# Performance work log

Hardware: AMD Instinct MI355X
Metric: run time of the kernel (lower is better)

## Reference

```python
import jax, jax.numpy as jnp
import numpy as np

B, S, D, H = 4, 2048, 1024, 16
HD = D // H
QMIN, QMAX = -128.0, 127.0


def fq(x):
    """Int8 per-tensor fake-quant (quantize-dequantize), straight-through."""
    s = jnp.maximum(jnp.max(jnp.abs(x)) / QMAX, 1e-8)
    q = jnp.clip(jnp.round(x / s), QMIN, QMAX) * s
    return x + jax.lax.stop_gradient(q - x)


def layernorm(x, g, b):
    m = jnp.mean(x, axis=-1, keepdims=True)
    v = jnp.var(x, axis=-1, keepdims=True)
    return (x - m) * jax.lax.rsqrt(v + 1e-5) * g + b


def rope(x):
    # x: [B, H, S, HD]; rotate-half RoPE
    half = HD // 2
    inv = 1.0 / (10000.0 ** (jnp.arange(half, dtype=jnp.float32) / half))
    ang = jnp.arange(S, dtype=jnp.float32)[:, None] * inv[None, :]  # [S, half]
    cos, sin = jnp.cos(ang), jnp.sin(ang)
    x1, x2 = x[..., :half], x[..., half:]
    return jnp.concatenate([x1 * cos - x2 * sin, x1 * sin + x2 * cos], axis=-1)


def setup_inputs() -> dict:
    key = jax.random.key(0)
    ks = jax.random.split(key, 16)
    w = lambda k, shp: jax.random.normal(k, shp, dtype=jnp.float32) * 0.02
    return {
        "x": jax.random.normal(ks[0], (B, S, D), dtype=jnp.float32),
        "g1": jnp.ones((D,), jnp.float32), "bn1": jnp.zeros((D,), jnp.float32),
        "Wq": w(ks[1], (D, D)), "bq": jnp.zeros((D,), jnp.float32),
        "Wk": w(ks[2], (D, D)), "bk": jnp.zeros((D,), jnp.float32),
        "Wv": w(ks[3], (D, D)), "bv": jnp.zeros((D,), jnp.float32),
        "Wo": w(ks[4], (D, D)), "bo": jnp.zeros((D,), jnp.float32),
        "g2": jnp.ones((D,), jnp.float32), "bn2": jnp.zeros((D,), jnp.float32),
        "W1": w(ks[5], (4 * D, D)), "bf1": jnp.zeros((4 * D,), jnp.float32),
        "W2": w(ks[6], (D, 4 * D)), "bf2": jnp.zeros((D,), jnp.float32),
    }


def reference(x, g1, bn1, Wq, bq, Wk, bk, Wv, bv, Wo, bo, g2, bn2, W1, bf1, W2, bf2):
    # --- attention branch: LN -> int8 quant -> RoPE MHSA -> quant add ---
    residual = x
    h = fq(layernorm(x, g1, bn1))  # post_norm1_quant
    q = h @ fq(Wq).T + bq
    k = h @ fq(Wk).T + bk
    v = h @ fq(Wv).T + bv
    q = rope(q.reshape(B, S, H, HD).transpose(0, 2, 1, 3))
    k = rope(k.reshape(B, S, H, HD).transpose(0, 2, 1, 3))
    v = v.reshape(B, S, H, HD).transpose(0, 2, 1, 3)
    scores = jnp.einsum("bhqd,bhkd->bhqk", q, k) / np.sqrt(HD).astype(np.float32)
    attn = jax.nn.softmax(scores, axis=-1)
    o = jnp.einsum("bhqk,bhkd->bhqd", attn, v)
    o = o.transpose(0, 2, 1, 3).reshape(B, S, D)
    o = fq(o @ fq(Wo).T + bo)  # attn returns quant tensor
    x = fq(o + residual)       # QuantAdd
    # --- MLP branch: LN -> quant -> fc1 -> GELU -> quant -> fc2 -> quant add ---
    residual = x
    h = fq(layernorm(x, g2, bn2))  # post_norm2_quant
    h = h @ fq(W1).T + bf1
    h = jax.nn.gelu(h, approximate=False)
    h = fq(h)                       # post_gelu_quant
    h = h @ fq(W2).T + bf2
    return fq(h + residual)         # QuantAdd
```

## Files before the change

### kernel.cpp

```cpp
#include <hip/hip_runtime.h>
#include <math.h>

#define Bdim 4
#define Sdim 2048
#define Ddim 1024
#define Hdim 16
#define HDdim 64

typedef unsigned long long u64;
typedef unsigned short ushort_t;
typedef int int4v __attribute__((ext_vector_type(4)));
typedef short short8v __attribute__((ext_vector_type(8)));
typedef float float4v __attribute__((ext_vector_type(4)));
typedef unsigned short us4v __attribute__((ext_vector_type(4)));

__device__ __forceinline__ float qdq_f(float x, float amax) {
  float s = fmaxf(amax / 127.0f, 1e-8f);
  float r = rintf(x / s);
  r = fminf(fmaxf(r, -128.0f), 127.0f);
  return r * s;
}

__device__ __forceinline__ void atomicMaxF(float* a, float v) {
  atomicMax((int*)a, __float_as_int(v));
}

__device__ __forceinline__ float blockMax256(float v) {
  __shared__ float sred[4];
  #pragma unroll
  for (int o = 32; o > 0; o >>= 1) v = fmaxf(v, __shfl_xor(v, o));
  if ((threadIdx.x & 63) == 0) sred[threadIdx.x >> 6] = v;
  __syncthreads();
  return fmaxf(fmaxf(sred[0], sred[1]), fmaxf(sred[2], sred[3]));
}

__device__ __forceinline__ ushort_t f2bf(float f) {
  unsigned u = __float_as_uint(f);
  return (ushort_t)((u + 0x7FFFu + ((u >> 16) & 1u)) >> 16);
}
__device__ __forceinline__ float bf2f(ushort_t h) {
  return __uint_as_float(((unsigned)h) << 16);
}

__global__ void init_scalars(float* s) { s[threadIdx.x] = 0.0f; }

__global__ __launch_bounds__(256) void absmax6_kernel(
    const float* __restrict__ Wq, const float* __restrict__ Wk,
    const float* __restrict__ Wv, const float* __restrict__ Wo,
    const float* __restrict__ W1, const float* __restrict__ W2,
    float* __restrict__ Sc)
{
  const u64 DD = (u64)Ddim * Ddim;
  int blk = blockIdx.x;
  const float* src; float* dst; u64 lb, nb, n;
  if (blk < 256)       { src = Wq; dst = Sc + 1; lb = blk;        nb = 256;  n = DD; }
  else if (blk < 512)  { src = Wk; dst = Sc + 2; lb = blk - 256;  nb = 256;  n = DD; }
  else if (blk < 768)  { src = Wv; dst = Sc + 3; lb = blk - 512;  nb = 256;  n = DD; }
  else if (blk < 1024) { src = Wo; dst = Sc + 4; lb = blk - 768;  nb = 256;  n = DD; }
  else if (blk < 2048) { src = W1; dst = Sc + 5; lb = blk - 1024; nb = 1024; n = 4 * DD; }
  else                 { src = W2; dst = Sc + 6; lb = blk - 2048; nb = 1024; n = 4 * DD; }
  u64 i = lb * 256 + threadIdx.x;
  u64 stride = nb * 256;
  float m = 0.0f;
  for (; i < n; i += stride) m = fmaxf(m, fabsf(src[i]));
  m = blockMax256(m);
  if (threadIdx.x == 0) atomicMaxF(dst, m);
}

__global__ __launch_bounds__(256) void quantw_kernel(
    const float* __restrict__ Wq, const float* __restrict__ Wk,
    const float* __restrict__ Wv, const float* __restrict__ Wo,
    const float* __restrict__ W1, const float* __restrict__ W2,
    signed char* __restrict__ Wq8, signed char* __restrict__ Wk8,
    signed char* __restrict__ Wv8, ushort_t* __restrict__ WoBF,
    signed char* __restrict__ W18, signed char* __restrict__ W28,
    const float* __restrict__ Sc)
{
  const u64 DD = (u64)Ddim * Ddim;
  int blk = blockIdx.x;
  if (blk < 2816) {
    const float* src; signed char* dst; float sa; u64 lb, nb, n4;
    if (blk < 256)       { src = Wq; dst = Wq8; sa = Sc[1]; lb = blk;        nb = 256;  n4 = DD / 4; }
    else if (blk < 512)  { src = Wk; dst = Wk8; sa = Sc[2]; lb = blk - 256;  nb = 256;  n4 = DD / 4; }
    else if (blk < 768)  { src = Wv; dst = Wv8; sa = Sc[3]; lb = blk - 512;  nb = 256;  n4 = DD / 4; }
    else if (blk < 1792) { src = W1; dst = W18; sa = Sc[5]; lb = blk - 768;  nb = 1024; n4 = DD; }
    else                 { src = W2; dst = W28; sa = Sc[6]; lb = blk - 1792; nb = 1024; n4 = DD; }
    const float s = fmaxf(sa / 127.0f, 1e-8f);
    u64 i = lb * 256 + threadIdx.x;
    u64 stride = nb * 256;
    for (; i < n4; i += stride) {
      float4 v = ((const float4*)src)[i];
      int b0 = (int)fminf(fmaxf(rintf(v.x / s), -128.0f), 127.0f) & 255;
      int b1 = (int)fminf(fmaxf(rintf(v.y / s), -128.0f), 127.0f) & 255;
      int b2 = (int)fminf(fmaxf(rintf(v.z / s), -128.0f), 127.0f) & 255;
      int b3 = (int)fminf(fmaxf(rintf(v.w / s), -128.0f), 127.0f) & 255;
      ((unsigned*)dst)[i] = (unsigned)(b0 | (b1 << 8) | (b2 << 16) | (b3 << 24));
    }
  } else {
    const float s = fmaxf(Sc[4] / 127.0f, 1e-8f);
    u64 i = (u64)(blk - 2816) * 256 + threadIdx.x;
    u64 stride = 1024ull * 256;
    for (; i < DD; i += stride) {
      float r = fminf(fmaxf(rintf(Wo[i] / s), -128.0f), 127.0f);
      WoBF[i] = f2bf(r);
    }
  }
}

__global__ __launch_bounds__(256) void quant8_kernel(
    const float* __restrict__ x, const float* __restrict__ amaxp,
    signed char* __restrict__ q, u64 n4)
{
  const float s = fmaxf(*amaxp / 127.0f, 1e-8f);
  u64 i = (u64)blockIdx.x * 256 + threadIdx.x;
  u64 stride = (u64)gridDim.x * 256;
  for (; i < n4; i += stride) {
    float4 v = ((const float4*)x)[i];
    int b0 = (int)fminf(fmaxf(rintf(v.x / s), -128.0f), 127.0f) & 255;
    int b1 = (int)fminf(fmaxf(rintf(v.y / s), -128.0f), 127.0f) & 255;
    int b2 = (int)fminf(fmaxf(rintf(v.z / s), -128.0f), 127.0f) & 255;
    int b3 = (int)fminf(fmaxf(rintf(v.w / s), -128.0f), 127.0f) & 255;
    ((unsigned*)q)[i] = (unsigned)(b0 | (b1 << 8) | (b2 << 16) | (b3 << 24));
  }
}

__global__ __launch_bounds__(256) void ln_kernel(
    const float* __restrict__ x, const float* __restrict__ g,
    const float* __restrict__ beta, const float* __restrict__ inAmax,
    float* __restrict__ y, float* __restrict__ amaxOut)
{
  __shared__ float sred[4];
  __shared__ float smv[2];
  const int tid = threadIdx.x;
  const u64 row = blockIdx.x;
  const float* xr = x + row * Ddim;
  float* yr = y + row * Ddim;
  float aIn = inAmax ? *inAmax : 0.0f;

  float vals[4];
  float sum = 0.0f;
  #pragma unroll
  for (int i = 0; i < 4; i++) {
    float v = xr[tid + (i << 8)];
    if (inAmax) v = qdq_f(v, aIn);
    vals[i] = v;
    sum += v;
  }
  #pragma unroll
  for (int o = 32; o > 0; o >>= 1) sum += __shfl_xor(sum, o);
  if ((tid & 63) == 0) sred[tid >> 6] = sum;
  __syncthreads();
  if (tid == 0) smv[0] = (sred[0] + sred[1] + sred[2] + sred[3]) * (1.0f / 1024.0f);
  __syncthreads();
  const float mean = smv[0];

  float dev = 0.0f;
  #pragma unroll
  for (int i = 0; i < 4; i++) { float d = vals[i] - mean; dev += d * d; }
  #pragma unroll
  for (int o = 32; o > 0; o >>= 1) dev += __shfl_xor(dev, o);
  if ((tid & 63) == 0) sred[tid >> 6] = dev;
  __syncthreads();
  if (tid == 0) {
    float var = (sred[0] + sred[1] + sred[2] + sred[3]) * (1.0f / 1024.0f);
    smv[1] = 1.0f / sqrtf(var + 1e-5f);
  }
  __syncthreads();
  const float inv = smv[1];

  float lmax = 0.0f;
  #pragma unroll
  for (int i = 0; i < 4; i++) {
    int c = tid + (i << 8);
    float ov = (vals[i] - mean) * inv * g[c] + beta[c];
    yr[c] = ov;
    lmax = fmaxf(lmax, fabsf(ov));
  }
  #pragma unroll
  for (int o = 32; o > 0; o >>= 1) lmax = fmaxf(lmax, __shfl_xor(lmax, o));
  __syncthreads();
  if ((tid & 63) == 0) sred[tid >> 6] = lmax;
  __syncthreads();
  if (tid == 0)
    atomicMaxF(amaxOut, fmaxf(fmaxf(sred[0], sred[1]), fmaxf(sred[2], sred[3])));
}

template <int EPI>
__global__ __launch_bounds__(256) void gemm_i8(
    const signed char* __restrict__ A8, const signed char* __restrict__ B8,
    const float* __restrict__ bias, float* __restrict__ C,
    int M, int N, int K,
    const float* __restrict__ sAp, const float* __restrict__ sBp,
    float* __restrict__ amaxOut,
    const float* __restrict__ Tm = nullptr,
    const float* __restrict__ amaxT = nullptr)
{
  __shared__ __align__(16) signed char As[128][80];
  __shared__ __align__(16) signed char Bs[128][80];
  const int tid = threadIdx.x;
  const int wave = tid >> 6, lane = tid & 63;
  const int quad = lane >> 4, l16 = lane & 15;
  const int wy = wave >> 1, wx = wave & 1;
  const int m0 = blockIdx.y << 7, n0 = blockIdx.x << 7;
  const float sA = fmaxf(*sAp / 127.0f, 1e-8f);
  const float sB = fmaxf(*sBp / 127.0f, 1e-8f);
  const float sAB = sA * sB;
  const float aT = (EPI == 2) ? *amaxT : 0.0f;

  const int sr = tid >> 2;
  const int sc = (tid & 3) << 4;

  int4v acc[4][4] = {};
  for (int k0 = 0; k0 < K; k0 += 64) {
    #pragma unroll
    for (int p = 0; p < 2; p++) {
      int r = sr + (p << 6);
      uint4 av = *(const uint4*)&A8[(u64)(m0 + r) * K + k0 + sc];
      uint4 bv = *(const uint4*)&B8[(u64)(n0 + r) * K + k0 + sc];
      *(uint4*)&As[r][sc] = av;
      *(uint4*)&Bs[r][sc] = bv;
    }
    __syncthreads();
    int4v af[4], bf[4];
    #pragma unroll
    for (int mt = 0; mt < 4; mt++)
      af[mt] = *(const int4v*)&As[(wy << 6) + (mt << 4) + l16][quad << 4];
    #pragma unroll
    for (int nt = 0; nt < 4; nt++)
      bf[nt] = *(const int4v*)&Bs[(wx << 6) + (nt << 4) + l16][quad << 4];
    #pragma unroll
    for (int mt = 0; mt < 4; mt++)
      #pragma unroll
      for (int nt = 0; nt < 4; nt++)
        acc[mt][nt] = __builtin_amdgcn_mfma_i32_16x16x64_i8(af[mt], bf[nt], acc[mt][nt], 0, 0, 0);
    __syncthreads();
  }

  float lmax = 0.0f;
  #pragma unroll
  for (int mt = 0; mt < 4; mt++) {
    #pragma unroll
    for (int reg = 0; reg < 4; reg++) {
      int row = m0 + (wy << 6) + (mt << 4) + (quad << 2) + reg;
      #pragma unroll
      for (int nt = 0; nt < 4; nt++) {
        int col = n0 + (wx << 6) + (nt << 4) + l16;
        float v = (float)acc[mt][nt][reg] * sAB + bias[col];
        if (EPI == 1) {
          v = 0.5f * v * (1.0f + erff(v * 0.70710678118654752440f));
          lmax = fmaxf(lmax, fabsf(v));
        }
        if (EPI == 2) {
          v += qdq_f(Tm[(u64)row * N + col], aT);
          lmax = fmaxf(lmax, fabsf(v));
        }
        C[(u64)row * N + col] = v;
      }
    }
  }
  if (EPI >= 1) {
    lmax = blockMax256(lmax);
    if (tid == 0) atomicMaxF(amaxOut, lmax);
  }
}

__global__ __launch_bounds__(256) void gemm_bf16_wo(
    const ushort_t* __restrict__ Ahi, const ushort_t* __restrict__ Alo,
    const ushort_t* __restrict__ Bw, const float* __restrict__ bias,
    float* __restrict__ C, int M, int N, int K,
    const float* __restrict__ sWp, float* __restrict__ amaxOut)
{
  __shared__ __align__(16) ushort_t Hs[128][40];
  __shared__ __align__(16) ushort_t Ls[128][40];
  __shared__ __align__(16) ushort_t Ws[128][40];
  const int tid = threadIdx.x;
  const int wave = tid >> 6, lane = tid & 63;
  const int quad = lane >> 4, l16 = lane & 15;
  const int wy = wave >> 1, wx = wave & 1;
  const int m0 = blockIdx.y << 7, n0 = blockIdx.x << 7;
  const float sW = fmaxf(*sWp / 127.0f, 1e-8f);

  const int sr = tid >> 2;
  const int sce = (tid & 3) << 3;

  float4v acc[4][4] = {};
  for (int k0 = 0; k0 < K; k0 += 32) {
    #pragma unroll
    for (int p = 0; p < 2; p++) {
      int r = sr + (p << 6);
      uint4 hv = *(const uint4*)&Ahi[(u64)(m0 + r) * K + k0 + sce];
      uint4 lv = *(const uint4*)&Alo[(u64)(m0 + r) * K + k0 + sce];
      uint4 wv = *(const uint4*)&Bw[(u64)(n0 + r) * K + k0 + sce];
      *(uint4*)&Hs[r][sce] = hv;
      *(uint4*)&Ls[r][sce] = lv;
      *(uint4*)&Ws[r][sce] = wv;
    }
    __syncthreads();
    short8v ah[4], al[4], bw[4];
    #pragma unroll
    for (int mt = 0; mt < 4; mt++) {
      ah[mt] = *(const short8v*)&Hs[(wy << 6) + (mt << 4) + l16][quad << 3];
      al[mt] = *(const short8v*)&Ls[(wy << 6) + (mt << 4) + l16][quad << 3];
    }
    #pragma unroll
    for (int nt = 0; nt < 4; nt++)
      bw[nt] = *(const short8v*)&Ws[(wx << 6) + (nt << 4) + l16][quad << 3];
    #pragma unroll
    for (int mt = 0; mt < 4; mt++)
      #pragma unroll
      for (int nt = 0; nt < 4; nt++) {
        acc[mt][nt] = __builtin_amdgcn_mfma_f32_16x16x32_bf16(ah[mt], bw[nt], acc[mt][nt], 0, 0, 0);
        acc[mt][nt] = __builtin_amdgcn_mfma_f32_16x16x32_bf16(al[mt], bw[nt], acc[mt][nt], 0, 0, 0);
      }
    __syncthreads();
  }

  float lmax = 0.0f;
  #pragma unroll
  for (int mt = 0; mt < 4; mt++) {
    #pragma unroll
    for (int reg = 0; reg < 4; reg++) {
      int row = m0 + (wy << 6) + (mt << 4) + (quad << 2) + reg;
      #pragma unroll
      for (int nt = 0; nt < 4; nt++) {
        int col = n0 + (wx << 6) + (nt << 4) + l16;
        float v = acc[mt][nt][reg] * sW + bias[col];
        lmax = fmaxf(lmax, fabsf(v));
        C[(u64)row * N + col] = v;
      }
    }
  }
  lmax = blockMax256(lmax);
  if (tid == 0) atomicMaxF(amaxOut, lmax);
}

__global__ __launch_bounds__(256) void prep_attn(
    const float* __restrict__ q, const float* __restrict__ k,
    const float* __restrict__ v,
    ushort_t* __restrict__ QH, ushort_t* __restrict__ QL,
    ushort_t* __restrict__ KH, ushort_t* __restrict__ KL,
    ushort_t* __restrict__ VTH, ushort_t* __restrict__ VTL,
    float* __restrict__ NQ, float* __restrict__ KMX)
{
  const int bh = blockIdx.y;
  const int b = bh >> 4, h = bh & 15;
  const int s0 = blockIdx.x << 6;
  const int tid = threadIdx.x;
  float kml = 0.0f;

  #pragma unroll
  for (int i = 0; i < 8; i++) {
    int idx = tid + (i << 8);
    int s = idx >> 5, hp = idx & 31;
    int sa = s0 + s;
    u64 gin = ((u64)(b * Sdim + sa) * Hdim + h) * HDdim + hp;
    float inv = powf(10000.0f, -(float)hp * (1.0f / 32.0f));
    float ang = (float)sa * inv;
    float cs = cosf(ang), sn = sinf(ang);
    float q1 = q[gin], q2 = q[gin + 32];
    float k1 = k[gin], k2 = k[gin + 32];
    float qo1 = (q1 * cs - q2 * sn) * 0.125f;
    float qo2 = (q1 * sn + q2 * cs) * 0.125f;
    float ko1 = k1 * cs - k2 * sn;
    float ko2 = k1 * sn + k2 * cs;
    u64 go = ((u64)bh * Sdim + sa) * HDdim + hp;
    ushort_t t;
    t = f2bf(qo1); QH[go]      = t; QL[go]      = f2bf(qo1 - bf2f(t));
    t = f2bf(qo2); QH[go + 32] = t; QL[go + 32] = f2bf(qo2 - bf2f(t));
    t = f2bf(ko1); KH[go]      = t; KL[go]      = f2bf(ko1 - bf2f(t));
    t = f2bf(ko2); KH[go + 32] = t; KL[go + 32] = f2bf(ko2 - bf2f(t));
    float nq2 = qo1 * qo1 + qo2 * qo2;
    float nk2 = ko1 * ko1 + ko2 * ko2;
    #pragma unroll
    for (int o = 16; o >= 1; o >>= 1) {
      nq2 += __shfl_xor(nq2, o);
      nk2 += __shfl_xor(nk2, o);
    }
    if (hp == 0) {
      NQ[(u64)bh * Sdim + sa] = sqrtf(nq2);
      kml = fmaxf(kml, sqrtf(nk2));
    }
  }
  kml = blockMax256(kml);
  if (tid == 0) atomicMaxF(&KMX[bh], kml);

  __shared__ ushort_t VHs[64][66], VLs[64][66];
  #pragma unroll
  for (int i = 0; i < 4; i++) {
    int idx4 = tid + (i << 8);
    int s = idx4 >> 4, c4 = (idx4 & 15) << 2;
    u64 gin = ((u64)(b * Sdim + s0 + s) * Hdim + h) * HDdim + c4;
    float4 vv = *(const float4*)&v[gin];
    float va[4] = {vv.x, vv.y, vv.z, vv.w};
    #pragma unroll
    for (int j = 0; j < 4; j++) {
      ushort_t vh = f2bf(va[j]);
      VHs[s][c4 + j] = vh;
      VLs[s][c4 + j] = f2bf(va[j] - bf2f(vh));
    }
  }
  __syncthreads();
  #pragma unroll
  for (int i = 0; i < 4; i++) {
    int idx4 = tid + (i << 8);
    int hd = idx4 >> 4, s4 = (idx4 & 15) << 2;
    us4v oh, ol;
    #pragma unroll
    for (int j = 0; j < 4; j++) { oh[j] = VHs[s4 + j][hd]; ol[j] = VLs[s4 + j][hd]; }
    u64 go = ((u64)bh * HDdim + hd) * Sdim + s0 + s4;
    *(us4v*)&VTH[go] = oh;
    *(us4v*)&VTL[go] = ol;
  }
}

__global__ __launch_bounds__(256) void attn_kernel(
    const ushort_t* __restrict__ QH, const ushort_t* __restrict__ QL,
    const ushort_t* __restrict__ KH, const ushort_t* __restrict__ KL,
    const ushort_t* __restrict__ VTH, const ushort_t* __restrict__ VTL,
    const float* __restrict__ NQ, const float* __restrict__ KMX,
    ushort_t* __restrict__ OHI, ushort_t* __restrict__ OLO)
{
  __shared__ __align__(16) ushort_t KHs[64][72], KLs[64][72];
  __shared__ __align__(16) ushort_t VHs[64][72], VLs[64][72];
  __shared__ __align__(16) float PF[128][68];
  const int tid = threadIdx.x;
  const int wave = tid >> 6, lane = tid & 63;
  const int quad = lane >> 4, l16 = lane & 15;
  const int w32 = wave << 5;
  const int bh = blockIdx.y;
  const int b = bh >> 4, h = bh & 15;
  const int q0 = blockIdx.x << 7;
  const u64 bhS = (u64)bh * Sdim;

  short8v qh[2][2], ql[2][2];
  #pragma unroll
  for (int mt = 0; mt < 2; mt++)
    #pragma unroll
    for (int kk = 0; kk < 2; kk++) {
      u64 g = (bhS + q0 + w32 + (mt << 4) + l16) * HDdim + (kk << 5) + (quad << 3);
      qh[mt][kk] = *(const short8v*)&QH[g];
      ql[mt][kk] = *(const short8v*)&QL[g];
    }

  const float kmax = KMX[bh] * 1.0009765625f;
  float Mb[2][4], lsum[2][4];
  #pragma unroll
  for (int mt = 0; mt < 2; mt++)
    #pragma unroll
    for (int r = 0; r < 4; r++) {
      Mb[mt][r] = NQ[bhS + q0 + w32 + (mt << 4) + (quad << 2) + r] * kmax;
      lsum[mt][r] = 0.0f;
    }

  float4v oacc[2][4] = {};

  for (int j0 = 0; j0 < Sdim; j0 += 64) {
    __syncthreads();
    #pragma unroll
    for (int i = 0; i < 2; i++) {
      int idx = tid + (i << 8);
      int r = idx >> 3, c8 = (idx & 7) << 3;
      u64 gk = (bhS + j0 + r) * HDdim + c8;
      *(uint4*)&KHs[r][c8] = *(const uint4*)&KH[gk];
      *(uint4*)&KLs[r][c8] = *(const uint4*)&KL[gk];
      u64 gv = ((u64)bh * HDdim + r) * Sdim + j0 + c8;
      *(uint4*)&VHs[r][c8] = *(const uint4*)&VTH[gv];
      *(uint4*)&VLs[r][c8] = *(const uint4*)&VTL[gv];
    }
    __syncthreads();

    float4v sc[2][4] = {};
    #pragma unroll
    for (int kk = 0; kk < 2; kk++)
      #pragma unroll
      for (int nt = 0; nt < 4; nt++) {
        short8v bh_ = *(const short8v*)&KHs[(nt << 4) + l16][(kk << 5) + (quad << 3)];
        short8v bl_ = *(const short8v*)&KLs[(nt << 4) + l16][(kk << 5) + (quad << 3)];
        #pragma unroll
        for (int mt = 0; mt < 2; mt++) {
          sc[mt][nt] = __builtin_amdgcn_mfma_f32_16x16x32_bf16(qh[mt][kk], bh_, sc[mt][nt], 0, 0, 0);
          sc[mt][nt] = __builtin_amdgcn_mfma_f32_16x16x32_bf16(qh[mt][kk], bl_, sc[mt][nt], 0, 0, 0);
          sc[mt][nt] = __builtin_amdgcn_mfma_f32_16x16x32_bf16(ql[mt][kk], bh_, sc[mt][nt], 0, 0, 0);
        }
      }

    #pragma unroll
    for (int mt = 0; mt < 2; mt++)
      #pragma unroll
      for (int r = 0; r < 4; r++) {
        int prow = w32 + (mt << 4) + (quad << 2) + r;
        float lacc = 0.0f;
        #pragma unroll
        for (int nt = 0; nt < 4; nt++) {
          float p = __expf(sc[mt][nt][r] - Mb[mt][r]);
          lacc += p;
          PF[prow][(nt << 4) + l16] = p;
        }
        lsum[mt][r] += lacc;
      }

    #pragma unroll
    for (int kk = 0; kk < 2; kk++) {
      short8v vh[4], vl[4];
      #pragma unroll
      for (int nt = 0; nt < 4; nt++) {
        vh[nt] = *(const short8v*)&VHs[(nt << 4) + l16][(kk << 5) + (quad << 3)];
        vl[nt] = *(const short8v*)&VLs[(nt << 4) + l16][(kk << 5) + (quad << 3)];
      }
      #pragma unroll
      for (int mt = 0; mt < 2; mt++) {
        const float* prp = &PF[w32 + (mt << 4) + l16][(kk << 5) + (quad << 3)];
        float4v pa = *(const float4v*)prp;
        float4v pb = *(const float4v*)(prp + 4);
        short8v ph, pl;
        #pragma unroll
        for (int j = 0; j < 4; j++) {
          unsigned ua = __float_as_uint(pa[j]);
          unsigned ub = __float_as_uint(pb[j]);
          float la = pa[j] - __uint_as_float(ua & 0xffff0000u);
          float lb = pb[j] - __uint_as_float(ub & 0xffff0000u);
          ph[j]     = (short)(ua >> 16);
          ph[4 + j] = (short)(ub >> 16);
          pl[j]     = (short)(__float_as_uint(la) >> 16);
          pl[4 + j] = (short)(__float_as_uint(lb) >> 16);
        }
        #pragma unroll
        for (int nt = 0; nt < 4; nt++) {
          oacc[mt][nt] = __builtin_amdgcn_mfma_f32_16x16x32_bf16(ph, vh[nt], oacc[mt][nt], 0, 0, 0);
          oacc[mt][nt] = __builtin_amdgcn_mfma_f32_16x16x32_bf16(ph, vl[nt], oacc[mt][nt], 0, 0, 0);
          oacc[mt][nt] = __builtin_amdgcn_mfma_f32_16x16x32_bf16(pl, vh[nt], oacc[mt][nt], 0, 0, 0);
        }
      }
    }
  }

  #pragma unroll
  for (int mt = 0; mt < 2; mt++)
    #pragma unroll
    for (int r = 0; r < 4; r++) {
      float l = lsum[mt][r];
      #pragma unroll
      for (int o = 8; o >= 1; o >>= 1) l += __shfl_xor(l, o);
      lsum[mt][r] = l;
    }

  #pragma unroll
  for (int mt = 0; mt < 2; mt++)
    #pragma unroll
    for (int r = 0; r < 4; r++) {
      float invl = 1.0f / lsum[mt][r];
      int srow = q0 + w32 + (mt << 4) + (quad << 2) + r;
      u64 gbase = ((u64)(b * Sdim + srow) * Hdim + h) * HDdim;
      #pragma unroll
      for (int nt = 0; nt < 4; nt++) {
        float o = oacc[mt][nt][r] * invl;
        ushort_t t = f2bf(o);
        OHI[gbase + (nt << 4) + l16] = t;
        OLO[gbase + (nt << 4) + l16] = f2bf(o - bf2f(t));
      }
    }
}

__global__ __launch_bounds__(256) void add_qdq_kernel(
    const float* __restrict__ a, const float* __restrict__ amaxA,
    const float* __restrict__ x, float* __restrict__ outp, u64 n,
    float* __restrict__ amaxOut)
{
  const float aA = *amaxA;
  u64 i = (u64)blockIdx.x * 256 + threadIdx.x;
  u64 stride = (u64)gridDim.x * 256;
  float m = 0.0f;
  for (; i < n; i += stride) {
    float t = qdq_f(a[i], aA) + x[i];
    outp[i] = t;
    m = fmaxf(m, fabsf(t));
  }
  m = blockMax256(m);
  if (threadIdx.x == 0) atomicMaxF(amaxOut, m);
}

__global__ __launch_bounds__(256) void qdq_out_kernel(
    const float* __restrict__ u, const float* __restrict__ amaxU,
    float* __restrict__ o, u64 n)
{
  const float aU = *amaxU;
  u64 i = (u64)blockIdx.x * 256 + threadIdx.x;
  u64 stride = (u64)gridDim.x * 256;
  for (; i < n; i += stride) o[i] = qdq_f(u[i], aU);
}

extern "C" void kernel_launch(void* const* d_in, const int* in_sizes, int n_in,
                              void* d_out, int out_size, void* d_ws, size_t ws_size,
                              hipStream_t stream)
{
  const float* x   = (const float*)d_in[0];
  const float* g1  = (const float*)d_in[1];
  const float* bn1 = (const float*)d_in[2];
  const float* Wq  = (const float*)d_in[3];
  const float* bq  = (const float*)d_in[4];
  const float* Wk  = (const float*)d_in[5];
  const float* bk  = (const float*)d_in[6];
  const float* Wv  = (const float*)d_in[7];
  const float* bv  = (const float*)d_in[8];
  const float* Wo  = (const float*)d_in[9];
  const float* bo  = (const float*)d_in[10];
  const float* g2  = (const float*)d_in[11];
  const float* bn2 = (const float*)d_in[12];
  const float* W1  = (const float*)d_in[13];
  const float* bf1 = (const float*)d_in[14];
  const float* W2  = (const float*)d_in[15];
  const float* bf2 = (const float*)d_in[16];
  float* out = (float*)d_out;

  const u64 NBSD = (u64)Bdim * Sdim * Ddim;
  const u64 NB4  = NBSD * 4;
  const u64 DD   = (u64)Ddim * Ddim;

  char* Wb = (char*)d_ws;
  float*       Sc   = (float*)Wb;
  float*       U0   = (float*)(Wb + 1024);
  float*       U1   = (float*)(Wb + 1024 + NB4);
  float*       F    = (float*)(Wb + 1024 + 2 * NB4);
  signed char* A8   = (signed char*)(Wb + 1024 + 6 * NB4);
  signed char* Wq8  = A8 + NBSD;
  signed char* Wk8  = Wq8 + DD;
  signed char* Wv8  = Wk8 + DD;
  signed char* W18  = Wv8 + DD;
  signed char* W28  = W18 + 4 * DD;
  ushort_t*    WoBF = (ushort_t*)(W28 + 4 * DD);
  float*       NQ   = (float*)(WoBF + DD);
  float*       KMX  = Sc + 128;

  float* F0 = F;
  float* F1 = F + NBSD;
  ushort_t* QHp = (ushort_t*)(F + 2 * NBSD);
  ushort_t* QLp = QHp + NBSD;
  ushort_t* KHp = (ushort_t*)(F + 3 * NBSD);
  ushort_t* KLp = KHp + NBSD;
  ushort_t* VTH = (ushort_t*)U0;
  ushort_t* VTL = VTH + NBSD;
  ushort_t* OHI = (ushort_t*)U1;
  ushort_t* OLO = OHI + NBSD;
  signed char* G8 = (signed char*)U0;

  const u64 needBytes = (u64)((char*)(NQ + (u64)64 * Sdim) - Wb);
  if (ws_size < needBytes) return;

  init_scalars<<<1, 256, 0, stream>>>(Sc);

  ln_kernel<<<Bdim * Sdim, 256, 0, stream>>>(x, g1, bn1, nullptr, U0, Sc + 0);

  absmax6_kernel<<<3072, 256, 0, stream>>>(Wq, Wk, Wv, Wo, W1, W2, Sc);

  quant8_kernel<<<4096, 256, 0, stream>>>(U0, Sc + 0, A8, NBSD / 4);
  quantw_kernel<<<3840, 256, 0, stream>>>(Wq, Wk, Wv, Wo, W1, W2,
                                          Wq8, Wk8, Wv8, WoBF, W18, W28, Sc);

  const int M = Bdim * Sdim;
  dim3 gP(Ddim / 128, M / 128);
  gemm_i8<0><<<gP, 256, 0, stream>>>(A8, Wq8, bq, U1, M, Ddim, Ddim, Sc + 0, Sc + 1, nullptr);
  gemm_i8<0><<<gP, 256, 0, stream>>>(A8, Wk8, bk, F0, M, Ddim, Ddim, Sc + 0, Sc + 2, nullptr);
  gemm_i8<0><<<gP, 256, 0, stream>>>(A8, Wv8, bv, F1, M, Ddim, Ddim, Sc + 0, Sc + 3, nullptr);

  dim3 gPrep(Sdim / 64, Bdim * Hdim);
  prep_attn<<<gPrep, 256, 0, stream>>>(U1, F0, F1, QHp, QLp, KHp, KLp, VTH, VTL, NQ, KMX);

  dim3 gAttn(Sdim / 128, Bdim * Hdim);
  attn_kernel<<<gAttn, 256, 0, stream>>>(QHp, QLp, KHp, KLp, VTH, VTL, NQ, KMX, OHI, OLO);

  gemm_bf16_wo<<<gP, 256, 0, stream>>>(OHI, OLO, WoBF, bo, F0, M, Ddim, Ddim, Sc + 4, Sc + 7);

  add_qdq_kernel<<<4096, 256, 0, stream>>>(F0, Sc + 7, x, U1, NBSD, Sc + 8);

  ln_kernel<<<Bdim * Sdim, 256, 0, stream>>>(U1, g2, bn2, Sc + 8, U0, Sc + 9);
  quant8_kernel<<<4096, 256, 0, stream>>>(U0, Sc + 9, A8, NBSD / 4);

  dim3 gF1(4 * Ddim / 128, M / 128);
  gemm_i8<1><<<gF1, 256, 0, stream>>>(A8, W18, bf1, F, M, 4 * Ddim, Ddim, Sc + 9, Sc + 5, Sc + 10);

  quant8_kernel<<<4096, 256, 0, stream>>>(F, Sc + 10, G8, NBSD);

  gemm_i8<2><<<gP, 256, 0, stream>>>(G8, W28, bf2, out, M, Ddim, 4 * Ddim,
                                     Sc + 10, Sc + 6, Sc + 11, U1, Sc + 8);

  qdq_out_kernel<<<4096, 256, 0, stream>>>(out, Sc + 11, out, NBSD);
}
```

Baseline: 1.184 ms.

## Fuse Q/K/V int8 GEMMs with RoPE, bf16 split and V transpose epilogue

```diff
diff --git a/kernel.cpp b/kernel.cpp
--- a/kernel.cpp
+++ b/kernel.cpp
@@ -85,23 +85,23 @@
     else if (blk < 768)  { src = Wv; dst = Wv8; sa = Sc[3]; lb = blk - 512;  nb = 256;  n4 = DD / 4; }
     else if (blk < 1792) { src = W1; dst = W18; sa = Sc[5]; lb = blk - 768;  nb = 1024; n4 = DD; }
     else                 { src = W2; dst = W28; sa = Sc[6]; lb = blk - 1792; nb = 1024; n4 = DD; }
-    const float s = fmaxf(sa / 127.0f, 1e-8f);
+    const float is = 1.0f / fmaxf(sa / 127.0f, 1e-8f);
     u64 i = lb * 256 + threadIdx.x;
     u64 stride = nb * 256;
     for (; i < n4; i += stride) {
       float4 v = ((const float4*)src)[i];
-      int b0 = (int)fminf(fmaxf(rintf(v.x / s), -128.0f), 127.0f) & 255;
-      int b1 = (int)fminf(fmaxf(rintf(v.y / s), -128.0f), 127.0f) & 255;
-      int b2 = (int)fminf(fmaxf(rintf(v.z / s), -128.0f), 127.0f) & 255;
-      int b3 = (int)fminf(fmaxf(rintf(v.w / s), -128.0f), 127.0f) & 255;
+      int b0 = (int)fminf(fmaxf(rintf(v.x * is), -128.0f), 127.0f) & 255;
+      int b1 = (int)fminf(fmaxf(rintf(v.y * is), -128.0f), 127.0f) & 255;
+      int b2 = (int)fminf(fmaxf(rintf(v.z * is), -128.0f), 127.0f) & 255;
+      int b3 = (int)fminf(fmaxf(rintf(v.w * is), -128.0f), 127.0f) & 255;
       ((unsigned*)dst)[i] = (unsigned)(b0 | (b1 << 8) | (b2 << 16) | (b3 << 24));
     }
   } else {
-    const float s = fmaxf(Sc[4] / 127.0f, 1e-8f);
+    const float is = 1.0f / fmaxf(Sc[4] / 127.0f, 1e-8f);
     u64 i = (u64)(blk - 2816) * 256 + threadIdx.x;
     u64 stride = 1024ull * 256;
     for (; i < DD; i += stride) {
-      float r = fminf(fmaxf(rintf(Wo[i] / s), -128.0f), 127.0f);
+      float r = fminf(fmaxf(rintf(Wo[i] * is), -128.0f), 127.0f);
       WoBF[i] = f2bf(r);
     }
   }
@@ -111,15 +111,15 @@
     const float* __restrict__ x, const float* __restrict__ amaxp,
     signed char* __restrict__ q, u64 n4)
 {
-  const float s = fmaxf(*amaxp / 127.0f, 1e-8f);
+  const float is = 1.0f / fmaxf(*amaxp / 127.0f, 1e-8f);
   u64 i = (u64)blockIdx.x * 256 + threadIdx.x;
   u64 stride = (u64)gridDim.x * 256;
   for (; i < n4; i += stride) {
     float4 v = ((const float4*)x)[i];
-    int b0 = (int)fminf(fmaxf(rintf(v.x / s), -128.0f), 127.0f) & 255;
-    int b1 = (int)fminf(fmaxf(rintf(v.y / s), -128.0f), 127.0f) & 255;
-    int b2 = (int)fminf(fmaxf(rintf(v.z / s), -128.0f), 127.0f) & 255;
-    int b3 = (int)fminf(fmaxf(rintf(v.w / s), -128.0f), 127.0f) & 255;
+    int b0 = (int)fminf(fmaxf(rintf(v.x * is), -128.0f), 127.0f) & 255;
+    int b1 = (int)fminf(fmaxf(rintf(v.y * is), -128.0f), 127.0f) & 255;
+    int b2 = (int)fminf(fmaxf(rintf(v.z * is), -128.0f), 127.0f) & 255;
+    int b3 = (int)fminf(fmaxf(rintf(v.w * is), -128.0f), 127.0f) & 255;
     ((unsigned*)q)[i] = (unsigned)(b0 | (b1 << 8) | (b2 << 16) | (b3 << 24));
   }
 }
@@ -264,6 +264,131 @@
   }
 }
 
+__global__ __launch_bounds__(256) void gemm_qkv(
+    const signed char* __restrict__ A8, const signed char* __restrict__ B8,
+    const float* __restrict__ bq, const float* __restrict__ bk,
+    const float* __restrict__ bv,
+    const float* __restrict__ Sc,
+    ushort_t* __restrict__ QH, ushort_t* __restrict__ QL,
+    ushort_t* __restrict__ KH, ushort_t* __restrict__ KL,
+    ushort_t* __restrict__ VTH, ushort_t* __restrict__ VTL,
+    float* __restrict__ NQ, float* __restrict__ KMX)
+{
+  __shared__ __align__(16) signed char As[128][80];
+  __shared__ __align__(16) signed char Bs[128][80];
+  const int tid = threadIdx.x;
+  const int wave = tid >> 6, lane = tid & 63;
+  const int quad = lane >> 4, l16 = lane & 15;
+  const int wy = wave >> 1, wx = wave & 1;
+  const int m0 = blockIdx.y << 7, n0 = blockIdx.x << 7;
+  const int K = Ddim;
+  const int seg = n0 >> 10;
+  const float sA = fmaxf(Sc[0] / 127.0f, 1e-8f);
+  const float sB = fmaxf(Sc[1 + seg] / 127.0f, 1e-8f);
+  const float sAB = sA * sB;
+  const float* bias = (seg == 0) ? bq : (seg == 1) ? bk : bv;
+  const int nseg = n0 - (seg << 10) + (wx << 6);
+  const int h = nseg >> 6;
+  const int bidx = m0 >> 11;
+  const int bh = (bidx << 4) + h;
+  const int bias_off = h << 6;
+
+  const int sr = tid >> 2;
+  const int sc_ = (tid & 3) << 4;
+
+  int4v acc[4][4] = {};
+  for (int k0 = 0; k0 < K; k0 += 64) {
+    #pragma unroll
+    for (int p = 0; p < 2; p++) {
+      int r = sr + (p << 6);
+      uint4 av = *(const uint4*)&A8[(u64)(m0 + r) * K + k0 + sc_];
+      uint4 bv_ = *(const uint4*)&B8[(u64)(n0 + r) * K + k0 + sc_];
+      *(uint4*)&As[r][sc_] = av;
+      *(uint4*)&Bs[r][sc_] = bv_;
+    }
+    __syncthreads();
+    int4v af[4], bf[4];
+    #pragma unroll
+    for (int mt = 0; mt < 4; mt++)
+      af[mt] = *(const int4v*)&As[(wy << 6) + (mt << 4) + l16][quad << 4];
+    #pragma unroll
+    for (int nt = 0; nt < 4; nt++)
+      bf[nt] = *(const int4v*)&Bs[(wx << 6) + (nt << 4) + l16][quad << 4];
+    #pragma unroll
+    for (int mt = 0; mt < 4; mt++)
+      #pragma unroll
+      for (int nt = 0; nt < 4; nt++)
+        acc[mt][nt] = __builtin_amdgcn_mfma_i32_16x16x64_i8(af[mt], bf[nt], acc[mt][nt], 0, 0, 0);
+    __syncthreads();
+  }
+
+  if (seg < 2) {
+    const float inv0 = powf(10000.0f, -(float)(l16) * (1.0f / 32.0f));
+    const float inv1 = powf(10000.0f, -(float)(16 + l16) * (1.0f / 32.0f));
+    ushort_t* OH = (seg == 0) ? QH : KH;
+    ushort_t* OL = (seg == 0) ? QL : KL;
+    const float qscale = (seg == 0) ? 0.125f : 1.0f;
+    float kml2 = 0.0f;
+    #pragma unroll
+    for (int mt = 0; mt < 4; mt++) {
+      #pragma unroll
+      for (int reg = 0; reg < 4; reg++) {
+        int row = m0 + (wy << 6) + (mt << 4) + (quad << 2) + reg;
+        int s = row & 2047;
+        u64 go = ((u64)bh * Sdim + s) * HDdim;
+        float nrm2 = 0.0f;
+        #pragma unroll
+        for (int nt = 0; nt < 2; nt++) {
+          int hp = (nt << 4) + l16;
+          float inv = nt ? inv1 : inv0;
+          float ang = (float)s * inv;
+          float cs = cosf(ang), sn = sinf(ang);
+          float x1 = (float)acc[mt][nt][reg] * sAB + bias[bias_off + hp];
+          float x2 = (float)acc[mt][nt + 2][reg] * sAB + bias[bias_off + hp + 32];
+          float o1 = (x1 * cs - x2 * sn) * qscale;
+          float o2 = (x1 * sn + x2 * cs) * qscale;
+          ushort_t t1 = f2bf(o1), t2 = f2bf(o2);
+          OH[go + hp]      = t1; OL[go + hp]      = f2bf(o1 - bf2f(t1));
+          OH[go + hp + 32] = t2; OL[go + hp + 32] = f2bf(o2 - bf2f(t2));
+          nrm2 += o1 * o1 + o2 * o2;
+        }
+        #pragma unroll
+        for (int o = 8; o >= 1; o >>= 1) nrm2 += __shfl_xor(nrm2, o);
+        if (seg == 0) {
+          if (l16 == 0) NQ[(u64)bh * Sdim + s] = sqrtf(nrm2);
+        } else {
+          kml2 = fmaxf(kml2, nrm2);
+        }
+      }
+    }
+    if (seg == 1) {
+      #pragma unroll
+      for (int o = 32; o >= 1; o >>= 1) kml2 = fmaxf(kml2, __shfl_xor(kml2, o));
+      if (lane == 0) atomicMaxF(&KMX[bh], sqrtf(kml2));
+    }
+  } else {
+    #pragma unroll
+    for (int mt = 0; mt < 4; mt++) {
+      int s_b = (m0 + (wy << 6) + (mt << 4) + (quad << 2)) & 2047;
+      #pragma unroll
+      for (int nt = 0; nt < 4; nt++) {
+        int hd = (nt << 4) + l16;
+        us4v oh, ol;
+        #pragma unroll
+        for (int reg = 0; reg < 4; reg++) {
+          float v = (float)acc[mt][nt][reg] * sAB + bias[bias_off + hd];
+          ushort_t t = f2bf(v);
+          oh[reg] = t;
+          ol[reg] = f2bf(v - bf2f(t));
+        }
+        u64 go = ((u64)bh * HDdim + hd) * Sdim + s_b;
+        *(us4v*)&VTH[go] = oh;
+        *(us4v*)&VTL[go] = ol;
+      }
+    }
+  }
+}
+
 __global__ __launch_bounds__(256) void gemm_bf16_wo(
     const ushort_t* __restrict__ Ahi, const ushort_t* __restrict__ Alo,
     const ushort_t* __restrict__ Bw, const float* __restrict__ bias,
@@ -332,85 +457,6 @@
   }
   lmax = blockMax256(lmax);
   if (tid == 0) atomicMaxF(amaxOut, lmax);
-}
-
-__global__ __launch_bounds__(256) void prep_attn(
-    const float* __restrict__ q, const float* __restrict__ k,
-    const float* __restrict__ v,
-    ushort_t* __restrict__ QH, ushort_t* __restrict__ QL,
-    ushort_t* __restrict__ KH, ushort_t* __restrict__ KL,
-    ushort_t* __restrict__ VTH, ushort_t* __restrict__ VTL,
-    float* __restrict__ NQ, float* __restrict__ KMX)
-{
-  const int bh = blockIdx.y;
-  const int b = bh >> 4, h = bh & 15;
-  const int s0 = blockIdx.x << 6;
-  const int tid = threadIdx.x;
-  float kml = 0.0f;
-
-  #pragma unroll
-  for (int i = 0; i < 8; i++) {
-    int idx = tid + (i << 8);
-    int s = idx >> 5, hp = idx & 31;
-    int sa = s0 + s;
-    u64 gin = ((u64)(b * Sdim + sa) * Hdim + h) * HDdim + hp;
-    float inv = powf(10000.0f, -(float)hp * (1.0f / 32.0f));
-    float ang = (float)sa * inv;
-    float cs = cosf(ang), sn = sinf(ang);
-    float q1 = q[gin], q2 = q[gin + 32];
-    float k1 = k[gin], k2 = k[gin + 32];
-    float qo1 = (q1 * cs - q2 * sn) * 0.125f;
-    float qo2 = (q1 * sn + q2 * cs) * 0.125f;
-    float ko1 = k1 * cs - k2 * sn;
-    float ko2 = k1 * sn + k2 * cs;
-    u64 go = ((u64)bh * Sdim + sa) * HDdim + hp;
-    ushort_t t;
-    t = f2bf(qo1); QH[go]      = t; QL[go]      = f2bf(qo1 - bf2f(t));
-    t = f2bf(qo2); QH[go + 32] = t; QL[go + 32] = f2bf(qo2 - bf2f(t));
-    t = f2bf(ko1); KH[go]      = t; KL[go]      = f2bf(ko1 - bf2f(t));
-    t = f2bf(ko2); KH[go + 32] = t; KL[go + 32] = f2bf(ko2 - bf2f(t));
-    float nq2 = qo1 * qo1 + qo2 * qo2;
-    float nk2 = ko1 * ko1 + ko2 * ko2;
-    #pragma unroll
-    for (int o = 16; o >= 1; o >>= 1) {
-      nq2 += __shfl_xor(nq2, o);
-      nk2 += __shfl_xor(nk2, o);
-    }
-    if (hp == 0) {
-      NQ[(u64)bh * Sdim + sa] = sqrtf(nq2);
-      kml = fmaxf(kml, sqrtf(nk2));
-    }
-  }
-  kml = blockMax256(kml);
-  if (tid == 0) atomicMaxF(&KMX[bh], kml);
-
-  __shared__ ushort_t VHs[64][66], VLs[64][66];
-  #pragma unroll
-  for (int i = 0; i < 4; i++) {
-    int idx4 = tid + (i << 8);
-    int s = idx4 >> 4, c4 = (idx4 & 15) << 2;
-    u64 gin = ((u64)(b * Sdim + s0 + s) * Hdim + h) * HDdim + c4;
-    float4 vv = *(const float4*)&v[gin];
-    float va[4] = {vv.x, vv.y, vv.z, vv.w};
-    #pragma unroll
-    for (int j = 0; j < 4; j++) {
-      ushort_t vh = f2bf(va[j]);
-      VHs[s][c4 + j] = vh;
-      VLs[s][c4 + j] = f2bf(va[j] - bf2f(vh));
-    }
-  }
-  __syncthreads();
-  #pragma unroll
-  for (int i = 0; i < 4; i++) {
-    int idx4 = tid + (i << 8);
-    int hd = idx4 >> 4, s4 = (idx4 & 15) << 2;
-    us4v oh, ol;
-    #pragma unroll
-    for (int j = 0; j < 4; j++) { oh[j] = VHs[s4 + j][hd]; ol[j] = VLs[s4 + j][hd]; }
-    u64 go = ((u64)bh * HDdim + hd) * Sdim + s0 + s4;
-    *(us4v*)&VTH[go] = oh;
-    *(us4v*)&VTL[go] = ol;
-  }
 }
 
 __global__ __launch_bounds__(256) void attn_kernel(
@@ -632,7 +678,6 @@
   float*       KMX  = Sc + 128;
 
   float* F0 = F;
-  float* F1 = F + NBSD;
   ushort_t* QHp = (ushort_t*)(F + 2 * NBSD);
   ushort_t* QLp = QHp + NBSD;
   ushort_t* KHp = (ushort_t*)(F + 3 * NBSD);
@@ -657,17 +702,15 @@
                                           Wq8, Wk8, Wv8, WoBF, W18, W28, Sc);
 
   const int M = Bdim * Sdim;
-  dim3 gP(Ddim / 128, M / 128);
-  gemm_i8<0><<<gP, 256, 0, stream>>>(A8, Wq8, bq, U1, M, Ddim, Ddim, Sc + 0, Sc + 1, nullptr);
-  gemm_i8<0><<<gP, 256, 0, stream>>>(A8, Wk8, bk, F0, M, Ddim, Ddim, Sc + 0, Sc + 2, nullptr);
-  gemm_i8<0><<<gP, 256, 0, stream>>>(A8, Wv8, bv, F1, M, Ddim, Ddim, Sc + 0, Sc + 3, nullptr);
-
-  dim3 gPrep(Sdim / 64, Bdim * Hdim);
-  prep_attn<<<gPrep, 256, 0, stream>>>(U1, F0, F1, QHp, QLp, KHp, KLp, VTH, VTL, NQ, KMX);
+
+  dim3 gQKV(3 * Ddim / 128, M / 128);
+  gemm_qkv<<<gQKV, 256, 0, stream>>>(A8, Wq8, bq, bk, bv, Sc,
+                                     QHp, QLp, KHp, KLp, VTH, VTL, NQ, KMX);
 
   dim3 gAttn(Sdim / 128, Bdim * Hdim);
   attn_kernel<<<gAttn, 256, 0, stream>>>(QHp, QLp, KHp, KLp, VTH, VTL, NQ, KMX, OHI, OLO);
 
+  dim3 gP(Ddim / 128, M / 128);
   gemm_bf16_wo<<<gP, 256, 0, stream>>>(OHI, OLO, WoBF, bo, F0, M, Ddim, Ddim, Sc + 4, Sc + 7);
 
   add_qdq_kernel<<<4096, 256, 0, stream>>>(F0, Sc + 7, x, U1, NBSD, Sc + 8);
```

Result: slower. 1.550 ms (+30.9%).

## Fuse Q/K/V int8 GEMMs into one launch and use reciprocal quant scales

Applied to the files above, without the earlier changes.

```diff
diff --git a/kernel.cpp b/kernel.cpp
--- a/kernel.cpp
+++ b/kernel.cpp
@@ -43,6 +43,12 @@
 }
 
 __global__ void init_scalars(float* s) { s[threadIdx.x] = 0.0f; }
+
+__global__ void bcat_kernel(const float* __restrict__ bq, const float* __restrict__ bk,
+                            const float* __restrict__ bv, float* __restrict__ o) {
+  int t = blockIdx.x * 256 + threadIdx.x;
+  o[t] = (t < 1024) ? bq[t] : (t < 2048) ? bk[t - 1024] : bv[t - 2048];
+}
 
 __global__ __launch_bounds__(256) void absmax6_kernel(
     const float* __restrict__ Wq, const float* __restrict__ Wk,
@@ -85,23 +91,23 @@
     else if (blk < 768)  { src = Wv; dst = Wv8; sa = Sc[3]; lb = blk - 512;  nb = 256;  n4 = DD / 4; }
     else if (blk < 1792) { src = W1; dst = W18; sa = Sc[5]; lb = blk - 768;  nb = 1024; n4 = DD; }
     else                 { src = W2; dst = W28; sa = Sc[6]; lb = blk - 1792; nb = 1024; n4 = DD; }
-    const float s = fmaxf(sa / 127.0f, 1e-8f);
+    const float is = 1.0f / fmaxf(sa / 127.0f, 1e-8f);
     u64 i = lb * 256 + threadIdx.x;
     u64 stride = nb * 256;
     for (; i < n4; i += stride) {
       float4 v = ((const float4*)src)[i];
-      int b0 = (int)fminf(fmaxf(rintf(v.x / s), -128.0f), 127.0f) & 255;
-      int b1 = (int)fminf(fmaxf(rintf(v.y / s), -128.0f), 127.0f) & 255;
-      int b2 = (int)fminf(fmaxf(rintf(v.z / s), -128.0f), 127.0f) & 255;
-      int b3 = (int)fminf(fmaxf(rintf(v.w / s), -128.0f), 127.0f) & 255;
+      int b0 = (int)fminf(fmaxf(rintf(v.x * is), -128.0f), 127.0f) & 255;
+      int b1 = (int)fminf(fmaxf(rintf(v.y * is), -128.0f), 127.0f) & 255;
+      int b2 = (int)fminf(fmaxf(rintf(v.z * is), -128.0f), 127.0f) & 255;
+      int b3 = (int)fminf(fmaxf(rintf(v.w * is), -128.0f), 127.0f) & 255;
       ((unsigned*)dst)[i] = (unsigned)(b0 | (b1 << 8) | (b2 << 16) | (b3 << 24));
     }
   } else {
-    const float s = fmaxf(Sc[4] / 127.0f, 1e-8f);
+    const float is = 1.0f / fmaxf(Sc[4] / 127.0f, 1e-8f);
     u64 i = (u64)(blk - 2816) * 256 + threadIdx.x;
     u64 stride = 1024ull * 256;
     for (; i < DD; i += stride) {
-      float r = fminf(fmaxf(rintf(Wo[i] / s), -128.0f), 127.0f);
+      float r = fminf(fmaxf(rintf(Wo[i] * is), -128.0f), 127.0f);
       WoBF[i] = f2bf(r);
     }
   }
@@ -111,15 +117,15 @@
     const float* __restrict__ x, const float* __restrict__ amaxp,
     signed char* __restrict__ q, u64 n4)
 {
-  const float s = fmaxf(*amaxp / 127.0f, 1e-8f);
+  const float is = 1.0f / fmaxf(*amaxp / 127.0f, 1e-8f);
   u64 i = (u64)blockIdx.x * 256 + threadIdx.x;
   u64 stride = (u64)gridDim.x * 256;
   for (; i < n4; i += stride) {
     float4 v = ((const float4*)x)[i];
-    int b0 = (int)fminf(fmaxf(rintf(v.x / s), -128.0f), 127.0f) & 255;
-    int b1 = (int)fminf(fmaxf(rintf(v.y / s), -128.0f), 127.0f) & 255;
-    int b2 = (int)fminf(fmaxf(rintf(v.z / s), -128.0f), 127.0f) & 255;
-    int b3 = (int)fminf(fmaxf(rintf(v.w / s), -128.0f), 127.0f) & 255;
+    int b0 = (int)fminf(fmaxf(rintf(v.x * is), -128.0f), 127.0f) & 255;
+    int b1 = (int)fminf(fmaxf(rintf(v.y * is), -128.0f), 127.0f) & 255;
+    int b2 = (int)fminf(fmaxf(rintf(v.z * is), -128.0f), 127.0f) & 255;
+    int b3 = (int)fminf(fmaxf(rintf(v.w * is), -128.0f), 127.0f) & 255;
     ((unsigned*)q)[i] = (unsigned)(b0 | (b1 << 8) | (b2 << 16) | (b3 << 24));
   }
 }
@@ -264,6 +270,67 @@
   }
 }
 
+__global__ __launch_bounds__(256) void gemm_qkv3(
+    const signed char* __restrict__ A8, const signed char* __restrict__ B8,
+    const float* __restrict__ bias, float* __restrict__ C,
+    const float* __restrict__ Sc)
+{
+  __shared__ __align__(16) signed char As[128][80];
+  __shared__ __align__(16) signed char Bs[128][80];
+  const int tid = threadIdx.x;
+  const int wave = tid >> 6, lane = tid & 63;
+  const int quad = lane >> 4, l16 = lane & 15;
+  const int wy = wave >> 1, wx = wave & 1;
+  const int m0 = blockIdx.y << 7, n0 = blockIdx.x << 7;
+  const int K = Ddim, N = 3 * Ddim;
+  const int seg = n0 >> 10;
+  const float sA = fmaxf(Sc[0] / 127.0f, 1e-8f);
+  const float sB = fmaxf(Sc[1 + seg] / 127.0f, 1e-8f);
+  const float sAB = sA * sB;
+
+  const int sr = tid >> 2;
+  const int sc_ = (tid & 3) << 4;
+
+  int4v acc[4][4] = {};
+  for (int k0 = 0; k0 < K; k0 += 64) {
+    #pragma unroll
+    for (int p = 0; p < 2; p++) {
+      int r = sr + (p << 6);
+      uint4 av = *(const uint4*)&A8[(u64)(m0 + r) * K + k0 + sc_];
+      uint4 bv = *(const uint4*)&B8[(u64)(n0 + r) * K + k0 + sc_];
+      *(uint4*)&As[r][sc_] = av;
+      *(uint4*)&Bs[r][sc_] = bv;
+    }
+    __syncthreads();
+    int4v af[4], bf[4];
+    #pragma unroll
+    for (int mt = 0; mt < 4; mt++)
+      af[mt] = *(const int4v*)&As[(wy << 6) + (mt << 4) + l16][quad << 4];
+    #pragma unroll
+    for (int nt = 0; nt < 4; nt++)
+      bf[nt] = *(const int4v*)&Bs[(wx << 6) + (nt << 4) + l16][quad << 4];
+    #pragma unroll
+    for (int mt = 0; mt < 4; mt++)
+      #pragma unroll
+      for (int nt = 0; nt < 4; nt++)
+        acc[mt][nt] = __builtin_amdgcn_mfma_i32_16x16x64_i8(af[mt], bf[nt], acc[mt][nt], 0, 0, 0);
+    __syncthreads();
+  }
+
+  #pragma unroll
+  for (int mt = 0; mt < 4; mt++) {
+    #pragma unroll
+    for (int reg = 0; reg < 4; reg++) {
+      int row = m0 + (wy << 6) + (mt << 4) + (quad << 2) + reg;
+      #pragma unroll
+      for (int nt = 0; nt < 4; nt++) {
+        int col = n0 + (wx << 6) + (nt << 4) + l16;
+        C[(u64)row * N + col] = (float)acc[mt][nt][reg] * sAB + bias[col];
+      }
+    }
+  }
+}
+
 __global__ __launch_bounds__(256) void gemm_bf16_wo(
     const ushort_t* __restrict__ Ahi, const ushort_t* __restrict__ Alo,
     const ushort_t* __restrict__ Bw, const float* __restrict__ bias,
@@ -335,8 +402,7 @@
 }
 
 __global__ __launch_bounds__(256) void prep_attn(
-    const float* __restrict__ q, const float* __restrict__ k,
-    const float* __restrict__ v,
+    const float* __restrict__ QKV,
     ushort_t* __restrict__ QH, ushort_t* __restrict__ QL,
     ushort_t* __restrict__ KH, ushort_t* __restrict__ KL,
     ushort_t* __restrict__ VTH, ushort_t* __restrict__ VTL,
@@ -353,12 +419,12 @@
     int idx = tid + (i << 8);
     int s = idx >> 5, hp = idx & 31;
     int sa = s0 + s;
-    u64 gin = ((u64)(b * Sdim + sa) * Hdim + h) * HDdim + hp;
+    u64 gin = (u64)(b * Sdim + sa) * 3072 + (h << 6) + hp;
     float inv = powf(10000.0f, -(float)hp * (1.0f / 32.0f));
     float ang = (float)sa * inv;
     float cs = cosf(ang), sn = sinf(ang);
-    float q1 = q[gin], q2 = q[gin + 32];
-    float k1 = k[gin], k2 = k[gin + 32];
+    float q1 = QKV[gin],        q2 = QKV[gin + 32];
+    float k1 = QKV[gin + 1024], k2 = QKV[gin + 1056];
     float qo1 = (q1 * cs - q2 * sn) * 0.125f;
     float qo2 = (q1 * sn + q2 * cs) * 0.125f;
     float ko1 = k1 * cs - k2 * sn;
@@ -389,8 +455,8 @@
   for (int i = 0; i < 4; i++) {
     int idx4 = tid + (i << 8);
     int s = idx4 >> 4, c4 = (idx4 & 15) << 2;
-    u64 gin = ((u64)(b * Sdim + s0 + s) * Hdim + h) * HDdim + c4;
-    float4 vv = *(const float4*)&v[gin];
+    u64 gin = (u64)(b * Sdim + s0 + s) * 3072 + 2048 + (h << 6) + c4;
+    float4 vv = *(const float4*)&QKV[gin];
     float va[4] = {vv.x, vv.y, vv.z, vv.w};
     #pragma unroll
     for (int j = 0; j < 4; j++) {
@@ -629,10 +695,11 @@
   signed char* W28  = W18 + 4 * DD;
   ushort_t*    WoBF = (ushort_t*)(W28 + 4 * DD);
   float*       NQ   = (float*)(WoBF + DD);
+  float*       BQKV = NQ + (u64)64 * Sdim;
   float*       KMX  = Sc + 128;
 
-  float* F0 = F;
-  float* F1 = F + NBSD;
+  float* QKV = U1;
+  float* F0  = F;
   ushort_t* QHp = (ushort_t*)(F + 2 * NBSD);
   ushort_t* QLp = QHp + NBSD;
   ushort_t* KHp = (ushort_t*)(F + 3 * NBSD);
@@ -643,10 +710,11 @@
   ushort_t* OLO = OHI + NBSD;
   signed char* G8 = (signed char*)U0;
 
-  const u64 needBytes = (u64)((char*)(NQ + (u64)64 * Sdim) - Wb);
+  const u64 needBytes = (u64)((char*)(BQKV + 3072) - Wb);
   if (ws_size < needBytes) return;
 
   init_scalars<<<1, 256, 0, stream>>>(Sc);
+  bcat_kernel<<<12, 256, 0, stream>>>(bq, bk, bv, BQKV);
 
   ln_kernel<<<Bdim * Sdim, 256, 0, stream>>>(x, g1, bn1, nullptr, U0, Sc + 0);
 
@@ -657,17 +725,17 @@
                                           Wq8, Wk8, Wv8, WoBF, W18, W28, Sc);
 
   const int M = Bdim * Sdim;
-  dim3 gP(Ddim / 128, M / 128);
-  gemm_i8<0><<<gP, 256, 0, stream>>>(A8, Wq8, bq, U1, M, Ddim, Ddim, Sc + 0, Sc + 1, nullptr);
-  gemm_i8<0><<<gP, 256, 0, stream>>>(A8, Wk8, bk, F0, M, Ddim, Ddim, Sc + 0, Sc + 2, nullptr);
-  gemm_i8<0><<<gP, 256, 0, stream>>>(A8, Wv8, bv, F1, M, Ddim, Ddim, Sc + 0, Sc + 3, nullptr);
+
+  dim3 gQKV(3 * Ddim / 128, M / 128);
+  gemm_qkv3<<<gQKV, 256, 0, stream>>>(A8, Wq8, BQKV, QKV, Sc);
 
   dim3 gPrep(Sdim / 64, Bdim * Hdim);
-  prep_attn<<<gPrep, 256, 0, stream>>>(U1, F0, F1, QHp, QLp, KHp, KLp, VTH, VTL, NQ, KMX);
+  prep_attn<<<gPrep, 256, 0, stream>>>(QKV, QHp, QLp, KHp, KLp, VTH, VTL, NQ, KMX);
 
   dim3 gAttn(Sdim / 128, Bdim * Hdim);
   attn_kernel<<<gAttn, 256, 0, stream>>>(QHp, QLp, KHp, KLp, VTH, VTL, NQ, KMX, OHI, OLO);
 
+  dim3 gP(Ddim / 128, M / 128);
   gemm_bf16_wo<<<gP, 256, 0, stream>>>(OHI, OLO, WoBF, bo, F0, M, Ddim, Ddim, Sc + 4, Sc + 7);
 
   add_qdq_kernel<<<4096, 256, 0, stream>>>(F0, Sc + 7, x, U1, NBSD, Sc + 8);
```

Result: faster. 1.075 ms (-9.2%).
